# Performance work log

Measured on AMD Instinct MI355X. Metric: run time of the kernel, lower is better.

## Reference

```python
import jax, jax.numpy as jnp
import numpy as np

B, S, D_MODEL, D_ATTN, H, F = 4, 2048, 512, 512, 8, 4
DEPTH = D_ATTN // H


def setup_inputs() -> dict:
    key = jax.random.key(0)
    ks = jax.random.split(key, 14)
    s = 0.02
    return {
        "q": jax.random.normal(ks[0], (B, S, D_MODEL), jnp.float32),
        "k": jax.random.normal(ks[1], (B, S, D_MODEL), jnp.float32),
        "v": jax.random.normal(ks[2], (B, S, D_MODEL), jnp.float32),
        "xdiff": jax.random.normal(ks[3], (B, S, S, F), jnp.float32),
        "wq": jax.random.normal(ks[4], (D_MODEL, D_ATTN), jnp.float32) * s,
        "bq": jnp.zeros((D_ATTN,), jnp.float32),
        "wk": jax.random.normal(ks[5], (D_MODEL, D_ATTN), jnp.float32) * s,
        "bk": jnp.zeros((D_ATTN,), jnp.float32),
        "wv": jax.random.normal(ks[6], (D_MODEL, D_ATTN), jnp.float32) * s,
        "bv": jnp.zeros((D_ATTN,), jnp.float32),
        "wx": jax.random.normal(ks[7], (D_ATTN, H * F), jnp.float32) * s,
        "bx": jnp.zeros((H * F,), jnp.float32),
        "wo": jax.random.normal(ks[8], (D_ATTN, D_MODEL), jnp.float32) * s,
        "bo": jnp.zeros((D_MODEL,), jnp.float32),
    }


def reference(q, k, v, xdiff, wq, bq, wk, bk, wv, bv, wx, bx, wo, bo):
    # projections
    qp = q @ wq + bq            # [B, Sq, D_ATTN]
    kp = k @ wk + bk            # [B, Sk, D_ATTN]
    vp = v @ wv + bv            # [B, Sk, D_ATTN]
    x = qp @ wx + bx            # [B, Sq, H*F]
    x = x.reshape(B, S, H, F)   # [B, Sq, H, F]

    # split heads -> [B, H, S, depth]
    def split_heads(t):
        return t.reshape(B, S, H, DEPTH).transpose(0, 2, 1, 3)

    qh, kh, vh = split_heads(qp), split_heads(kp), split_heads(vp)

    # xdiff bias: [B, Sq, Sk, F] x [B, Sq, H, F] -> [B, H, Sq, Sk]
    bias = jnp.einsum('bqkf,bqhf->bhqk', xdiff, x) / jnp.sqrt(jnp.float32(F))

    logits = jnp.einsum('bhqd,bhkd->bhqk', qh, kh) / jnp.sqrt(jnp.float32(DEPTH)) + bias
    attn = jax.nn.softmax(logits, axis=-1)              # [B, H, Sq, Sk]
    out = jnp.einsum('bhqk,bhkd->bhqd', attn, vh)       # [B, H, Sq, depth]
    out = out.transpose(0, 2, 1, 3).reshape(B, S, D_ATTN)
    out = out @ wo + bo                                  # [B, Sq, D_MODEL]
    return out, attn
```

## Files before the change

### kernel.cpp

```cpp
#include <hip/hip_runtime.h>
#include <stdint.h>

#define S_LEN 2048
#define NB 4
#define NH 8

typedef __attribute__((ext_vector_type(8))) short s8v;
typedef __attribute__((ext_vector_type(4))) float f4v;

#define MFMA16(a, b, c) __builtin_amdgcn_mfma_f32_16x16x32_bf16((a), (b), (c), 0, 0, 0)

static __device__ __forceinline__ unsigned short f2bf(float f) {
    unsigned int u = __builtin_bit_cast(unsigned int, f);
    u += 0x7fffu + ((u >> 16) & 1u);
    return (unsigned short)(u >> 16);
}
static __device__ __forceinline__ float bf2f(unsigned short h) {
    unsigned int u = ((unsigned int)h) << 16;
    return __builtin_bit_cast(float, u);
}

template <int MODE, bool ABF16>
__global__ __launch_bounds__(256) void gemm_tile(
    const void* __restrict__ Av, const float* __restrict__ W,
    const float* __restrict__ bias, void* __restrict__ Cv)
{
    __shared__ unsigned short a_lds[64 * 32];
    __shared__ unsigned short wt_lds[64 * 32];
    const int t = threadIdx.x;
    const int w = t >> 6, lane = t & 63;
    const int quad = lane >> 4, l15 = lane & 15;
    const int m0 = blockIdx.x * 64, n0 = blockIdx.y * 64;

    f4v acc[4] = {};

    const int srow = t >> 2, sc8 = (t & 3) * 8;
    const int wkk = t >> 3, wnn = (t & 7) * 8;

    for (int k0 = 0; k0 < 512; k0 += 32) {
        __syncthreads();
        if constexpr (ABF16) {
            const unsigned short* ap =
                (const unsigned short*)Av + (size_t)(m0 + srow) * 512 + k0 + sc8;
            *(uint4*)&a_lds[srow * 32 + sc8] = *(const uint4*)ap;
        } else {
            const float* ap = (const float*)Av + (size_t)(m0 + srow) * 512 + k0 + sc8;
            f4v v0 = *(const f4v*)ap;
            f4v v1 = *(const f4v*)(ap + 4);
            *(ushort4*)&a_lds[srow * 32 + sc8] =
                make_ushort4(f2bf(v0[0]), f2bf(v0[1]), f2bf(v0[2]), f2bf(v0[3]));
            *(ushort4*)&a_lds[srow * 32 + sc8 + 4] =
                make_ushort4(f2bf(v1[0]), f2bf(v1[1]), f2bf(v1[2]), f2bf(v1[3]));
        }
        {
            const float* wp = W + (size_t)(k0 + wkk) * 512 + n0 + wnn;
            f4v a0 = *(const f4v*)wp;
            f4v a1 = *(const f4v*)(wp + 4);
            #pragma unroll
            for (int i = 0; i < 4; ++i) wt_lds[(wnn + i) * 32 + wkk] = f2bf(a0[i]);
            #pragma unroll
            for (int i = 0; i < 4; ++i) wt_lds[(wnn + 4 + i) * 32 + wkk] = f2bf(a1[i]);
        }
        __syncthreads();
        s8v wf = *(const s8v*)&wt_lds[(w * 16 + l15) * 32 + quad * 8];
        #pragma unroll
        for (int rt = 0; rt < 4; ++rt) {
            s8v af = *(const s8v*)&a_lds[(rt * 16 + l15) * 32 + quad * 8];
            acc[rt] = MFMA16(af, wf, acc[rt]);
        }
    }

    const float bv = bias[n0 + w * 16 + l15];
    const int n = n0 + w * 16 + l15;
    #pragma unroll
    for (int rt = 0; rt < 4; ++rt) {
        const int mb = m0 + rt * 16 + quad * 4;
        if constexpr (MODE == 0) {
            unsigned short* C = (unsigned short*)Cv;
            #pragma unroll
            for (int r = 0; r < 4; ++r)
                C[(size_t)(mb + r) * 512 + n] = f2bf(acc[rt][r] + bv);
        } else if constexpr (MODE == 1) {
            unsigned short* C = (unsigned short*)Cv;
            ushort4 u = make_ushort4(f2bf(acc[rt][0] + bv), f2bf(acc[rt][1] + bv),
                                     f2bf(acc[rt][2] + bv), f2bf(acc[rt][3] + bv));
            *(ushort4*)&C[(size_t)(mb >> 11) * (512 * 2048) + (size_t)n * 2048 + (mb & 2047)] = u;
        } else {
            float* C = (float*)Cv;
            #pragma unroll
            for (int r = 0; r < 4; ++r)
                C[(size_t)(mb + r) * 512 + n] = acc[rt][r] + bv;
        }
    }
}

__global__ __launch_bounds__(256) void xproj_kernel(
    const unsigned short* __restrict__ qp, const float* __restrict__ wx,
    const float* __restrict__ bx, float* __restrict__ xout)
{
    __shared__ unsigned short qrow[8 * 512];
    const int t = threadIdx.x;
    const size_t base = (size_t)blockIdx.x * 8 * 512;
    #pragma unroll
    for (int i = 0; i < 2; ++i) {
        const int idx = (i * 256 + t) * 8;
        *(uint4*)&qrow[idx] = *(const uint4*)&qp[base + idx];
    }
    __syncthreads();
    const int r = t >> 5, j = t & 31;
    float acc = bx[j];
    #pragma unroll 8
    for (int d = 0; d < 512; ++d)
        acc = fmaf(bf2f(qrow[r * 512 + d]), wx[d * 32 + j], acc);
    xout[(size_t)blockIdx.x * 256 + t] = acc;
}

__global__ __launch_bounds__(256) void attn_kernel(
    const unsigned short* __restrict__ qp, const unsigned short* __restrict__ kp,
    const unsigned short* __restrict__ vT, const float* __restrict__ xws,
    const float* __restrict__ xdiff, float* __restrict__ attn,
    unsigned short* __restrict__ obuf)
{
    __shared__ float x_lds[16 * 32];
    __shared__ unsigned short p_lds[4 * 2 * 16 * 32];
    const int t = threadIdx.x, w = t >> 6, lane = t & 63;
    const int quad = lane >> 4, l15 = lane & 15;
    const int b = blockIdx.y, q0 = blockIdx.x * 16;
    const int h0 = 2 * w;

    {
        const float* src = xws + ((size_t)(b * S_LEN) + q0) * 32;
        x_lds[t] = src[t];
        x_lds[t + 256] = src[t + 256];
    }
    __syncthreads();

    s8v qf[2][2];
    #pragma unroll
    for (int e = 0; e < 2; ++e)
        #pragma unroll
        for (int kk = 0; kk < 2; ++kk)
            qf[e][kk] = *(const s8v*)&qp[((size_t)(b * S_LEN + q0 + l15)) * 512 +
                                         (h0 + e) * 64 + kk * 32 + quad * 8];

    f4v xh[2][4];
    #pragma unroll
    for (int e = 0; e < 2; ++e)
        #pragma unroll
        for (int r = 0; r < 4; ++r)
            xh[e][r] = *(const f4v*)&x_lds[(quad * 4 + r) * 32 + (h0 + e) * 4];

    const size_t kp_base = (size_t)b * S_LEN * 512;
    const size_t xd_base = ((size_t)(b * S_LEN) + q0) * S_LEN * 4;
    const size_t vt_base = (size_t)b * 512 * S_LEN;

    float lpart[2][4] = {};

    for (int k0 = 0; k0 < S_LEN; k0 += 32) {
        s8v kf[2][2][2];
        #pragma unroll
        for (int e = 0; e < 2; ++e)
            #pragma unroll
            for (int kt = 0; kt < 2; ++kt)
                #pragma unroll
                for (int kk = 0; kk < 2; ++kk)
                    kf[e][kt][kk] = *(const s8v*)&kp[kp_base +
                        (size_t)(k0 + kt * 16 + l15) * 512 + (h0 + e) * 64 + kk * 32 + quad * 8];
        f4v xd[2][4];
        #pragma unroll
        for (int kt = 0; kt < 2; ++kt)
            #pragma unroll
            for (int r = 0; r < 4; ++r)
                xd[kt][r] = *(const f4v*)&xdiff[xd_base +
                    ((size_t)(quad * 4 + r) * S_LEN + k0 + kt * 16 + l15) * 4];

        #pragma unroll
        for (int e = 0; e < 2; ++e) {
            #pragma unroll
            for (int kt = 0; kt < 2; ++kt) {
                f4v c = {0.f, 0.f, 0.f, 0.f};
                c = MFMA16(qf[e][0], kf[e][kt][0], c);
                c = MFMA16(qf[e][1], kf[e][kt][1], c);
                #pragma unroll
                for (int r = 0; r < 4; ++r) {
                    float bias4 = xd[kt][r][0] * xh[e][r][0] + xd[kt][r][1] * xh[e][r][1] +
                                  xd[kt][r][2] * xh[e][r][2] + xd[kt][r][3] * xh[e][r][3];
                    float lg = c[r] * 0.125f + bias4 * 0.5f;
                    lpart[e][r] += __expf(lg);
                }
            }
        }
    }

    float rinv[2][4];
    #pragma unroll
    for (int e = 0; e < 2; ++e)
        #pragma unroll
        for (int r = 0; r < 4; ++r) {
            float s = lpart[e][r];
            s += __shfl_xor(s, 1);
            s += __shfl_xor(s, 2);
            s += __shfl_xor(s, 4);
            s += __shfl_xor(s, 8);
            rinv[e][r] = 1.0f / s;
        }

    f4v oacc[2][4] = {};
    for (int k0 = 0; k0 < S_LEN; k0 += 32) {
        s8v kf[2][2][2];
        #pragma unroll
        for (int e = 0; e < 2; ++e)
            #pragma unroll
            for (int kt = 0; kt < 2; ++kt)
                #pragma unroll
                for (int kk = 0; kk < 2; ++kk)
                    kf[e][kt][kk] = *(const s8v*)&kp[kp_base +
                        (size_t)(k0 + kt * 16 + l15) * 512 + (h0 + e) * 64 + kk * 32 + quad * 8];
        f4v xd[2][4];
        #pragma unroll
        for (int kt = 0; kt < 2; ++kt)
            #pragma unroll
            for (int r = 0; r < 4; ++r)
                xd[kt][r] = *(const f4v*)&xdiff[xd_base +
                    ((size_t)(quad * 4 + r) * S_LEN + k0 + kt * 16 + l15) * 4];

        #pragma unroll
        for (int e = 0; e < 2; ++e) {
            #pragma unroll
            for (int kt = 0; kt < 2; ++kt) {
                f4v c = {0.f, 0.f, 0.f, 0.f};
                c = MFMA16(qf[e][0], kf[e][kt][0], c);
                c = MFMA16(qf[e][1], kf[e][kt][1], c);
                #pragma unroll
                for (int r = 0; r < 4; ++r) {
                    float bias4 = xd[kt][r][0] * xh[e][r][0] + xd[kt][r][1] * xh[e][r][1] +
                                  xd[kt][r][2] * xh[e][r][2] + xd[kt][r][3] * xh[e][r][3];
                    float lg = c[r] * 0.125f + bias4 * 0.5f;
                    float P = __expf(lg) * rinv[e][r];
                    size_t aidx = ((size_t)((b * NH + h0 + e) * S_LEN) + q0 + quad * 4 + r) * S_LEN +
                                  k0 + kt * 16 + l15;
                    __builtin_nontemporal_store(P, &attn[aidx]);
                    p_lds[((w * 2 + e) * 16 + quad * 4 + r) * 32 + kt * 16 + l15] = f2bf(P);
                }
            }
            s8v pa = *(const s8v*)&p_lds[((w * 2 + e) * 16 + l15) * 32 + quad * 8];
            #pragma unroll
            for (int dt = 0; dt < 4; ++dt) {
                s8v vf = *(const s8v*)&vT[vt_base +
                    (size_t)((h0 + e) * 64 + dt * 16 + l15) * S_LEN + k0 + quad * 8];
                oacc[e][dt] = MFMA16(pa, vf, oacc[e][dt]);
            }
        }
    }

    #pragma unroll
    for (int e = 0; e < 2; ++e)
        #pragma unroll
        for (int dt = 0; dt < 4; ++dt)
            #pragma unroll
            for (int r = 0; r < 4; ++r)
                obuf[((size_t)(b * S_LEN + q0 + quad * 4 + r)) * 512 +
                     (h0 + e) * 64 + dt * 16 + l15] = f2bf(oacc[e][dt][r]);
}

extern "C" void kernel_launch(void* const* d_in, const int* in_sizes, int n_in,
                              void* d_out, int out_size, void* d_ws, size_t ws_size,
                              hipStream_t stream) {
    const float* q     = (const float*)d_in[0];
    const float* k     = (const float*)d_in[1];
    const float* v     = (const float*)d_in[2];
    const float* xdiff = (const float*)d_in[3];
    const float* wq    = (const float*)d_in[4];
    const float* bq    = (const float*)d_in[5];
    const float* wk    = (const float*)d_in[6];
    const float* bk    = (const float*)d_in[7];
    const float* wv    = (const float*)d_in[8];
    const float* bv    = (const float*)d_in[9];
    const float* wx    = (const float*)d_in[10];
    const float* bx    = (const float*)d_in[11];
    const float* wo    = (const float*)d_in[12];
    const float* bo    = (const float*)d_in[13];

    float* outp = (float*)d_out;
    float* attn = outp + (size_t)NB * S_LEN * 512;

    const size_t MK = (size_t)8192 * 512;
    unsigned short* qp   = (unsigned short*)d_ws;
    unsigned short* kpw  = qp + MK;
    unsigned short* vT   = kpw + MK;
    unsigned short* obuf = vT + MK;
    float* xws = (float*)(obuf + MK);

    dim3 gg(128, 8);
    gemm_tile<0, false><<<gg, 256, 0, stream>>>(q, wq, bq, qp);
    gemm_tile<0, false><<<gg, 256, 0, stream>>>(k, wk, bk, kpw);
    gemm_tile<1, false><<<gg, 256, 0, stream>>>(v, wv, bv, vT);
    xproj_kernel<<<1024, 256, 0, stream>>>(qp, wx, bx, xws);
    attn_kernel<<<dim3(128, 4), 256, 0, stream>>>(qp, kpw, vT, xws, xdiff, attn, obuf);
    gemm_tile<2, true><<<gg, 256, 0, stream>>>(obuf, wo, bo, outp);
}
```

Before: 1.358 ms.

## Split attention over key chunks and pre-transpose weights to bf16

The single attention kernel becomes two kernels. One computes partial softmax denominators over 4 key chunks; the other does the PV pass over 2 key chunks and writes fp32 partial outputs. The output GEMM then sums the two partials while loading A. This raises the grid from 512 blocks to 2048 and 1024, to fill the GPU's CUs. Separately, the weights are transposed and converted to bf16 once by a prep kernel, so GEMM tiles load them with plain vector copies instead of strided LDS scatter writes. The cost is extra launches, fp32 partial-output traffic, and reloading the q fragments for each chunk.

Result: no change. 1.360 ms (+0.1%).

```diff
diff --git a/kernel.cpp b/kernel.cpp
--- a/kernel.cpp
+++ b/kernel.cpp
@@ -4,6 +4,8 @@
 #define S_LEN 2048
 #define NB 4
 #define NH 8
+#define KC_A 4
+#define KC_B 2
 
 typedef __attribute__((ext_vector_type(8))) short s8v;
 typedef __attribute__((ext_vector_type(4))) float f4v;
@@ -20,9 +22,20 @@
     return __builtin_bit_cast(float, u);
 }
 
-template <int MODE, bool ABF16>
+__global__ __launch_bounds__(256) void wprep(const float* __restrict__ W,
+                                             unsigned short* __restrict__ Wt)
+{
+    __shared__ float tile[16][17];
+    const int tx = threadIdx.x, ty = threadIdx.y;
+    const int n0 = blockIdx.x * 16, k0 = blockIdx.y * 16;
+    tile[ty][tx] = W[(size_t)(k0 + ty) * 512 + n0 + tx];
+    __syncthreads();
+    Wt[(size_t)(n0 + ty) * 512 + k0 + tx] = f2bf(tile[tx][ty]);
+}
+
+template <int MODE, int ASRC>
 __global__ __launch_bounds__(256) void gemm_tile(
-    const void* __restrict__ Av, const float* __restrict__ W,
+    const void* __restrict__ Av, const unsigned short* __restrict__ Wt,
     const float* __restrict__ bias, void* __restrict__ Cv)
 {
     __shared__ unsigned short a_lds[64 * 32];
@@ -33,17 +46,11 @@
     const int m0 = blockIdx.x * 64, n0 = blockIdx.y * 64;
 
     f4v acc[4] = {};
-
     const int srow = t >> 2, sc8 = (t & 3) * 8;
-    const int wkk = t >> 3, wnn = (t & 7) * 8;
 
     for (int k0 = 0; k0 < 512; k0 += 32) {
         __syncthreads();
-        if constexpr (ABF16) {
-            const unsigned short* ap =
-                (const unsigned short*)Av + (size_t)(m0 + srow) * 512 + k0 + sc8;
-            *(uint4*)&a_lds[srow * 32 + sc8] = *(const uint4*)ap;
-        } else {
+        if constexpr (ASRC == 0) {
             const float* ap = (const float*)Av + (size_t)(m0 + srow) * 512 + k0 + sc8;
             f4v v0 = *(const f4v*)ap;
             f4v v1 = *(const f4v*)(ap + 4);
@@ -51,16 +58,18 @@
                 make_ushort4(f2bf(v0[0]), f2bf(v0[1]), f2bf(v0[2]), f2bf(v0[3]));
             *(ushort4*)&a_lds[srow * 32 + sc8 + 4] =
                 make_ushort4(f2bf(v1[0]), f2bf(v1[1]), f2bf(v1[2]), f2bf(v1[3]));
-        }
-        {
-            const float* wp = W + (size_t)(k0 + wkk) * 512 + n0 + wnn;
-            f4v a0 = *(const f4v*)wp;
-            f4v a1 = *(const f4v*)(wp + 4);
-            #pragma unroll
-            for (int i = 0; i < 4; ++i) wt_lds[(wnn + i) * 32 + wkk] = f2bf(a0[i]);
-            #pragma unroll
-            for (int i = 0; i < 4; ++i) wt_lds[(wnn + 4 + i) * 32 + wkk] = f2bf(a1[i]);
-        }
+        } else {
+            const float* a0 = (const float*)Av + (size_t)(m0 + srow) * 512 + k0 + sc8;
+            const float* a1 = a0 + (size_t)8192 * 512;
+            f4v v0 = *(const f4v*)a0 + *(const f4v*)a1;
+            f4v v1 = *(const f4v*)(a0 + 4) + *(const f4v*)(a1 + 4);
+            *(ushort4*)&a_lds[srow * 32 + sc8] =
+                make_ushort4(f2bf(v0[0]), f2bf(v0[1]), f2bf(v0[2]), f2bf(v0[3]));
+            *(ushort4*)&a_lds[srow * 32 + sc8 + 4] =
+                make_ushort4(f2bf(v1[0]), f2bf(v1[1]), f2bf(v1[2]), f2bf(v1[3]));
+        }
+        *(uint4*)&wt_lds[srow * 32 + sc8] =
+            *(const uint4*)(Wt + (size_t)(n0 + srow) * 512 + k0 + sc8);
         __syncthreads();
         s8v wf = *(const s8v*)&wt_lds[(w * 16 + l15) * 32 + quad * 8];
         #pragma unroll
@@ -115,17 +124,15 @@
     xout[(size_t)blockIdx.x * 256 + t] = acc;
 }
 
-__global__ __launch_bounds__(256) void attn_kernel(
+__global__ __launch_bounds__(256) void attn_sums(
     const unsigned short* __restrict__ qp, const unsigned short* __restrict__ kp,
-    const unsigned short* __restrict__ vT, const float* __restrict__ xws,
-    const float* __restrict__ xdiff, float* __restrict__ attn,
-    unsigned short* __restrict__ obuf)
+    const float* __restrict__ xws, const float* __restrict__ xdiff,
+    float* __restrict__ lpart)
 {
     __shared__ float x_lds[16 * 32];
-    __shared__ unsigned short p_lds[4 * 2 * 16 * 32];
     const int t = threadIdx.x, w = t >> 6, lane = t & 63;
     const int quad = lane >> 4, l15 = lane & 15;
-    const int b = blockIdx.y, q0 = blockIdx.x * 16;
+    const int b = blockIdx.y, q0 = blockIdx.x * 16, kc = blockIdx.z;
     const int h0 = 2 * w;
 
     {
@@ -142,7 +149,6 @@
         for (int kk = 0; kk < 2; ++kk)
             qf[e][kk] = *(const s8v*)&qp[((size_t)(b * S_LEN + q0 + l15)) * 512 +
                                          (h0 + e) * 64 + kk * 32 + quad * 8];
-
     f4v xh[2][4];
     #pragma unroll
     for (int e = 0; e < 2; ++e)
@@ -152,11 +158,10 @@
 
     const size_t kp_base = (size_t)b * S_LEN * 512;
     const size_t xd_base = ((size_t)(b * S_LEN) + q0) * S_LEN * 4;
-    const size_t vt_base = (size_t)b * 512 * S_LEN;
-
-    float lpart[2][4] = {};
-
-    for (int k0 = 0; k0 < S_LEN; k0 += 32) {
+
+    float lp[2][4] = {};
+    const int kbeg = kc * (S_LEN / KC_A);
+    for (int k0 = kbeg; k0 < kbeg + S_LEN / KC_A; k0 += 32) {
         s8v kf[2][2][2];
         #pragma unroll
         for (int e = 0; e < 2; ++e)
@@ -186,27 +191,80 @@
                     float bias4 = xd[kt][r][0] * xh[e][r][0] + xd[kt][r][1] * xh[e][r][1] +
                                   xd[kt][r][2] * xh[e][r][2] + xd[kt][r][3] * xh[e][r][3];
                     float lg = c[r] * 0.125f + bias4 * 0.5f;
-                    lpart[e][r] += __expf(lg);
+                    lp[e][r] += __expf(lg);
                 }
             }
         }
     }
 
-    float rinv[2][4];
     #pragma unroll
     for (int e = 0; e < 2; ++e)
         #pragma unroll
         for (int r = 0; r < 4; ++r) {
-            float s = lpart[e][r];
+            float s = lp[e][r];
             s += __shfl_xor(s, 1);
             s += __shfl_xor(s, 2);
             s += __shfl_xor(s, 4);
             s += __shfl_xor(s, 8);
+            if (l15 == 0)
+                lpart[(((size_t)kc * NB + b) * NH + h0 + e) * S_LEN + q0 + quad * 4 + r] = s;
+        }
+}
+
+__global__ __launch_bounds__(256) void attn_pv(
+    const unsigned short* __restrict__ qp, const unsigned short* __restrict__ kp,
+    const unsigned short* __restrict__ vT, const float* __restrict__ xws,
+    const float* __restrict__ xdiff, const float* __restrict__ lpart,
+    float* __restrict__ attn, float* __restrict__ opart)
+{
+    __shared__ float x_lds[16 * 32];
+    __shared__ unsigned short p_lds[4 * 2 * 16 * 32];
+    const int t = threadIdx.x, w = t >> 6, lane = t & 63;
+    const int quad = lane >> 4, l15 = lane & 15;
+    const int b = blockIdx.y, q0 = blockIdx.x * 16, kcb = blockIdx.z;
+    const int h0 = 2 * w;
+
+    {
+        const float* src = xws + ((size_t)(b * S_LEN) + q0) * 32;
+        x_lds[t] = src[t];
+        x_lds[t + 256] = src[t + 256];
+    }
+    __syncthreads();
+
+    s8v qf[2][2];
+    #pragma unroll
+    for (int e = 0; e < 2; ++e)
+        #pragma unroll
+        for (int kk = 0; kk < 2; ++kk)
+            qf[e][kk] = *(const s8v*)&qp[((size_t)(b * S_LEN + q0 + l15)) * 512 +
+                                         (h0 + e) * 64 + kk * 32 + quad * 8];
+    f4v xh[2][4];
+    #pragma unroll
+    for (int e = 0; e < 2; ++e)
+        #pragma unroll
+        for (int r = 0; r < 4; ++r)
+            xh[e][r] = *(const f4v*)&x_lds[(quad * 4 + r) * 32 + (h0 + e) * 4];
+
+    const size_t kp_base = (size_t)b * S_LEN * 512;
+    const size_t xd_base = ((size_t)(b * S_LEN) + q0) * S_LEN * 4;
+    const size_t vt_base = (size_t)b * 512 * S_LEN;
+
+    float rinv[2][4];
+    #pragma unroll
+    for (int e = 0; e < 2; ++e)
+        #pragma unroll
+        for (int r = 0; r < 4; ++r) {
+            const int row = q0 + quad * 4 + r;
+            float s = 0.f;
+            #pragma unroll
+            for (int kc = 0; kc < KC_A; ++kc)
+                s += lpart[(((size_t)kc * NB + b) * NH + h0 + e) * S_LEN + row];
             rinv[e][r] = 1.0f / s;
         }
 
     f4v oacc[2][4] = {};
-    for (int k0 = 0; k0 < S_LEN; k0 += 32) {
+    const int kbeg = kcb * (S_LEN / KC_B);
+    for (int k0 = kbeg; k0 < kbeg + S_LEN / KC_B; k0 += 32) {
         s8v kf[2][2][2];
         #pragma unroll
         for (int e = 0; e < 2; ++e)
@@ -259,8 +317,8 @@
         for (int dt = 0; dt < 4; ++dt)
             #pragma unroll
             for (int r = 0; r < 4; ++r)
-                obuf[((size_t)(b * S_LEN + q0 + quad * 4 + r)) * 512 +
-                     (h0 + e) * 64 + dt * 16 + l15] = f2bf(oacc[e][dt][r]);
+                opart[((size_t)kcb * 8192 + b * S_LEN + q0 + quad * 4 + r) * 512 +
+                      (h0 + e) * 64 + dt * 16 + l15] = oacc[e][dt][r];
 }
 
 extern "C" void kernel_launch(void* const* d_in, const int* in_sizes, int n_in,
@@ -285,17 +343,32 @@
     float* attn = outp + (size_t)NB * S_LEN * 512;
 
     const size_t MK = (size_t)8192 * 512;
+    const size_t WSZ = (size_t)512 * 512;
     unsigned short* qp   = (unsigned short*)d_ws;
     unsigned short* kpw  = qp + MK;
     unsigned short* vT   = kpw + MK;
-    unsigned short* obuf = vT + MK;
-    float* xws = (float*)(obuf + MK);
+    unsigned short* wtq  = vT + MK;
+    unsigned short* wtk  = wtq + WSZ;
+    unsigned short* wtv  = wtk + WSZ;
+    unsigned short* wto  = wtv + WSZ;
+    float* xws   = (float*)(wto + WSZ);
+    float* lpart = xws + (size_t)8192 * 32;
+    float* opart = lpart + (size_t)KC_A * NB * NH * S_LEN;
+
+    dim3 wg(32, 32), wb(16, 16);
+    wprep<<<wg, wb, 0, stream>>>(wq, wtq);
+    wprep<<<wg, wb, 0, stream>>>(wk, wtk);
+    wprep<<<wg, wb, 0, stream>>>(wv, wtv);
+    wprep<<<wg, wb, 0, stream>>>(wo, wto);
 
     dim3 gg(128, 8);
-    gemm_tile<0, false><<<gg, 256, 0, stream>>>(q, wq, bq, qp);
-    gemm_tile<0, false><<<gg, 256, 0, stream>>>(k, wk, bk, kpw);
-    gemm_tile<1, false><<<gg, 256, 0, stream>>>(v, wv, bv, vT);
+    gemm_tile<0, 0><<<gg, 256, 0, stream>>>(q, wtq, bq, qp);
+    gemm_tile<0, 0><<<gg, 256, 0, stream>>>(k, wtk, bk, kpw);
+    gemm_tile<1, 0><<<gg, 256, 0, stream>>>(v, wtv, bv, vT);
     xproj_kernel<<<1024, 256, 0, stream>>>(qp, wx, bx, xws);
-    attn_kernel<<<dim3(128, 4), 256, 0, stream>>>(qp, kpw, vT, xws, xdiff, attn, obuf);
-    gemm_tile<2, true><<<gg, 256, 0, stream>>>(obuf, wo, bo, outp);
-}
+
+    attn_sums<<<dim3(128, NB, KC_A), 256, 0, stream>>>(qp, kpw, xws, xdiff, lpart);
+    attn_pv<<<dim3(128, NB, KC_B), 256, 0, stream>>>(qp, kpw, vT, xws, xdiff, lpart, attn, opart);
+
+    gemm_tile<2, 2><<<gg, 256, 0, stream>>>(opart, wto, bo, outp);
+}
```
